# Kernel optimization log

Measured on AMD Instinct MI355X. Metric: run time of the kernel, lower is better.

The kernel has to match this reference:

```python
import jax, jax.numpy as jnp
import numpy as np

WS = 7          # window size
DIM = 192
HEADS = 6
NW = 64         # number of windows per image (mask leading dim)
NC = 3          # n_contrast (q and kv)
B_ = 1024       # num_windows * batch


def _relative_position_index(ws):
    coords = np.stack(np.meshgrid(np.arange(ws), np.arange(ws), indexing='ij'))  # (2, ws, ws)
    cf = coords.reshape(2, -1)                       # (2, ws*ws)
    rel = cf[:, :, None] - cf[:, None, :]            # (2, N, N)
    rel = rel.transpose(1, 2, 0).copy()              # (N, N, 2)
    rel[:, :, 0] += ws - 1
    rel[:, :, 1] += ws - 1
    rel[:, :, 0] *= 2 * ws - 1
    return rel.sum(-1)                               # (N, N) int

REL_IDX = jnp.asarray(_relative_position_index(WS))


def setup_inputs() -> dict:
    key = jax.random.key(0)
    ks = jax.random.split(key, 13)
    f32 = jnp.float32
    inp = {
        'x_q': jax.random.normal(ks[0], (B_, NC, WS, WS, DIM), f32),
        'x_k': jax.random.normal(ks[1], (B_, NC, WS, WS, DIM), f32),
        'x_v': jax.random.normal(ks[2], (B_, NC, WS, WS, DIM), f32),
        'mask': jax.random.normal(ks[3], (NW, WS * WS, WS * WS), f32),
        # Linear weights stored torch-style: (out_features, in_features)
        'q_w': jax.random.normal(ks[4], (DIM, DIM), f32) * 0.02,
        'q_b': jnp.zeros((DIM,), f32),
        'k_w': jax.random.normal(ks[5], (DIM, DIM), f32) * 0.02,
        'k_b': jnp.zeros((DIM,), f32),
        'v_w': jax.random.normal(ks[6], (DIM, DIM), f32) * 0.02,
        'v_b': jnp.zeros((DIM,), f32),
        'proj_w': jax.random.normal(ks[7], (DIM, DIM), f32) * 0.02,
        'proj_b': jnp.zeros((DIM,), f32),
        'bias_table': jax.random.normal(ks[8], ((2 * WS - 1) ** 2, HEADS), f32) * 0.02,
    }
    return inp


def reference(x_q, x_k, x_v, mask, q_w, q_b, k_w, k_b, v_w, v_b, proj_w, proj_b, bias_table):
    Bw, ncq, Wh, Ww, C = x_q.shape
    nckv = x_k.shape[1]
    H = HEADS
    hd = C // H
    Nq = ncq * Wh * Ww
    Nkv = nckv * Wh * Ww

    xq = x_q.reshape(Bw, Nq, C)
    xk = x_k.reshape(Bw, Nkv, C)
    xv = x_v.reshape(Bw, Nkv, C)

    q = (xq @ q_w.T + q_b).reshape(Bw, Nq, H, hd).transpose(0, 2, 1, 3)   # (B_, H, Nq, hd)
    k = (xk @ k_w.T + k_b).reshape(Bw, Nkv, H, hd).transpose(0, 2, 1, 3)
    v = (xv @ v_w.T + v_b).reshape(Bw, Nkv, H, hd).transpose(0, 2, 1, 3)

    scale = hd ** (-0.5)
    attn = jnp.einsum('bhqd,bhkd->bhqk', q * scale, k)                    # (B_, H, Nq, Nkv)

    Nwin = Wh * Ww
    bias = bias_table[REL_IDX.reshape(-1)].reshape(Nwin, Nwin, H)
    bias = bias.transpose(2, 0, 1)                                        # (H, Nwin, Nwin)
    bias = jnp.tile(bias, (1, ncq, nckv))                                 # (H, Nq, Nkv)
    attn = attn + bias[None]

    nW = mask.shape[0]
    m = jnp.tile(mask, (1, ncq, nckv))                                    # (nW, Nq, Nkv)
    attn = attn.reshape(Bw // nW, nW, H, Nq, Nkv) + m[None, :, None]
    attn = attn.reshape(Bw, H, Nq, Nkv)
    attn = jax.nn.softmax(attn, axis=-1)

    out = jnp.einsum('bhqk,bhkd->bhqd', attn, v)                          # (B_, H, Nq, hd)
    out = out.transpose(0, 2, 1, 3).reshape(Bw, Nq, C)
    out = out @ proj_w.T + proj_b
    return out.reshape(Bw, ncq, Wh, Ww, C)
```

## Files before the change

### kernel.cpp

```cpp
#include <hip/hip_runtime.h>
#include <stdint.h>

#define ROWS 150528
#define QSCALE 0.17677669529663687f
#define L2E 1.44269504088896f

typedef __attribute__((ext_vector_type(8))) __bf16 bf16x8;
typedef __attribute__((ext_vector_type(4))) __bf16 bf16x4;
typedef __attribute__((ext_vector_type(4))) float f32x4;
typedef __attribute__((ext_vector_type(4))) float f4;

static __device__ __forceinline__ f32x4 mfma_bf16(bf16x8 a, bf16x8 b, f32x4 c) {
  return __builtin_amdgcn_mfma_f32_16x16x32_bf16(a, b, c, 0, 0, 0);
}

static __device__ __forceinline__ uint32_t pack_bf16(float a, float b) {
  uint16_t ux = __builtin_bit_cast(uint16_t, (__bf16)a);
  uint16_t uy = __builtin_bit_cast(uint16_t, (__bf16)b);
  return (uint32_t)ux | ((uint32_t)uy << 16);
}

#define GLOAD_LDS16(gp, lp)                                                     \
  __builtin_amdgcn_global_load_lds(                                             \
      (const __attribute__((address_space(1))) uint32_t*)(gp),                  \
      (__attribute__((address_space(3))) uint32_t*)(lp), 16, 0, 0)

__global__ void prep(const float* __restrict__ q_w, const float* __restrict__ k_w,
                     const float* __restrict__ v_w, const float* __restrict__ p_w,
                     __bf16* __restrict__ wq, __bf16* __restrict__ wk,
                     __bf16* __restrict__ wv, __bf16* __restrict__ wp,
                     const float* __restrict__ maskp, const float* __restrict__ btab,
                     float* __restrict__ bmall) {
  const int bid = blockIdx.x;
  if (bid < 144) {
    const int y = bid / 36;
    const float* s = y == 0 ? q_w : y == 1 ? k_w : y == 2 ? v_w : p_w;
    __bf16* d = y == 0 ? wq : y == 1 ? wk : y == 2 ? wv : wp;
    int i = (bid % 36) * 256 + threadIdx.x;
    f4 v = ((const f4*)s)[i];
    bf16x4 b;
    b[0] = (__bf16)v[0]; b[1] = (__bf16)v[1]; b[2] = (__bf16)v[2]; b[3] = (__bf16)v[3];
    ((bf16x4*)d)[i] = b;
  } else {
    const int idx = bid - 144;
    const int win = idx / 6, h = idx - win * 6;
    float* dst = bmall + ((size_t)idx) * 2800;
    for (int i = threadIdx.x; i < 2796; i += 256) {
      int q = i / 57, ke = i - q * 57;
      int k = ke >= 49 ? ke - 49 : ke;
      if (q > 48) q = 48;
      int qi = q / 7, qj = q - qi * 7, ki = k / 7, kj = k - ki * 7;
      int rel = (qi - ki + 6) * 13 + (qj - kj + 6);
      dst[i] = (maskp[win * 2401 + q * 49 + k] + btab[rel * 6 + h]) * L2E;
    }
  }
}

template<bool IN_F32, bool OUT_F32, int RPT, int TILES>
static __device__ __forceinline__
void gemm_pipe(const void* __restrict__ Xv, const __bf16* __restrict__ Wb,
               const float* __restrict__ bias, void* __restrict__ Ov, float scale,
               char* Xs)
{
  constexpr int CPR = IN_F32 ? 48 : 24;
  constexpr int LPW = RPT * CPR / 256;
  constexpr int TB  = RPT * CPR * 16;
  constexpr int RG  = RPT / 16;
  constexpr int STEADY = RG * 12 + LPW;
  const int tid = threadIdx.x;
  const int wv = tid >> 6, lane = tid & 63, lr = lane & 15, lg = lane >> 4;
  const size_t blk0 = (size_t)blockIdx.x * (RPT * TILES);

  bf16x8 wf[3][6];
  float bcol[3];
  #pragma unroll
  for (int t = 0; t < 3; ++t) {
    const int nt = wv + 4 * t;
    const __bf16* wr = &Wb[(nt * 16 + lr) * 192 + lg * 8];
    #pragma unroll
    for (int kk = 0; kk < 6; ++kk) wf[t][kk] = *(const bf16x8*)&wr[kk * 32];
    bcol[t] = bias[nt * 16 + lr] * scale;
  }

  auto stage = [&](int buf, int t) {
    const size_t row0 = blk0 + (size_t)t * RPT;
    char* ldsb = Xs + buf * TB;
    int l = (wv * LPW) * 64 + lane;
    #pragma unroll
    for (int p = 0; p < LPW; ++p) {
      int r = l / CPR;
      int c16 = (l - r * CPR) ^ (r & 7);
      const char* src;
      if (IN_F32) {
        src = (const char*)Xv + ((row0 + r) * 768 + c16 * 16);
      } else {
        int hh = c16 >> 2, sub = c16 & 3;
        src = (const char*)Xv + (((size_t)hh * ROWS + row0 + r) * 64 + sub * 16);
      }
      GLOAD_LDS16(src, ldsb + (wv * LPW + p) * 1024);
      l += 64;
    }
  };

  stage(0, 0);
  stage(1, 1);

  #pragma unroll
  for (int it = 0; it < TILES; ++it) {
    if (it == 0) {
      asm volatile("s_waitcnt vmcnt(%0)" :: "i"(LPW) : "memory");
    } else if (it + 1 < TILES) {
      asm volatile("s_waitcnt vmcnt(%0)" :: "i"(STEADY) : "memory");
    } else {
      asm volatile("s_waitcnt vmcnt(0)" ::: "memory");
    }
    __builtin_amdgcn_s_barrier();

    const size_t row0 = blk0 + (size_t)it * RPT;
    const char* cb = Xs + (it % 3) * TB;

    bf16x8 a[RG][6];
    #pragma unroll
    for (int rg = 0; rg < RG; ++rg) {
      const int rr = rg * 16 + lr;
      const char* rb = cb + rr * (CPR * 16);
      const int sw = rr & 7;
      if (IN_F32) {
        #pragma unroll
        for (int kk = 0; kk < 6; ++kk) {
          const int g0 = kk * 8 + lg * 2;
          f4 lo = *(const f4*)(rb + ((g0 ^ sw) * 16));
          f4 hi = *(const f4*)(rb + (((g0 + 1) ^ sw) * 16));
          #pragma unroll
          for (int e = 0; e < 4; ++e) {
            a[rg][kk][e]     = (__bf16)lo[e];
            a[rg][kk][4 + e] = (__bf16)hi[e];
          }
        }
      } else {
        #pragma unroll
        for (int kk = 0; kk < 6; ++kk) {
          const int g = kk * 4 + lg;
          a[rg][kk] = *(const bf16x8*)(rb + ((g ^ sw) * 16));
        }
      }
    }

    if (it + 2 < TILES) stage((it + 2) % 3, it + 2);
    asm volatile("" ::: "memory");

    #pragma unroll
    for (int rg = 0; rg < RG; ++rg) {
      const size_t grow = row0 + rg * 16 + lg * 4;
      #pragma unroll
      for (int t = 0; t < 3; ++t) {
        f32x4 acc = {0.f, 0.f, 0.f, 0.f};
        #pragma unroll
        for (int kk = 0; kk < 6; ++kk) acc = mfma_bf16(a[rg][kk], wf[t][kk], acc);
        const int nt = wv + 4 * t;
        if (OUT_F32) {
          const int col = nt * 16 + lr;
          #pragma unroll
          for (int j = 0; j < 4; ++j)
            ((float*)Ov)[(grow + j) * 192 + col] = acc[j] * scale + bcol[t];
        } else {
          const int hh = nt >> 1, c32 = (nt & 1) * 16 + lr;
          #pragma unroll
          for (int j = 0; j < 4; ++j)
            ((__bf16*)Ov)[((size_t)hh * ROWS + grow + j) * 32 + c32] =
                (__bf16)(acc[j] * scale + bcol[t]);
        }
      }
    }
    asm volatile("" ::: "memory");
  }
}

__global__ __launch_bounds__(256, 2)
void qkvgemm(const float* __restrict__ xq, const float* __restrict__ xk,
             const float* __restrict__ xv,
             const __bf16* __restrict__ wq, const __bf16* __restrict__ wk,
             const __bf16* __restrict__ wv,
             const float* __restrict__ bq, const float* __restrict__ bk,
             const float* __restrict__ bv,
             __bf16* __restrict__ oq, __bf16* __restrict__ ok,
             __bf16* __restrict__ ov)
{
  __shared__ __align__(16) char Xs[3 * 12288];
  const int y = blockIdx.y;
  const float* x = y == 0 ? xq : y == 1 ? xk : xv;
  const __bf16* w = y == 0 ? wq : y == 1 ? wk : wv;
  const float* bi = y == 0 ? bq : y == 1 ? bk : bv;
  __bf16* o = y == 0 ? oq : y == 1 ? ok : ov;
  const float scale = y == 0 ? (QSCALE * L2E) : 1.f;
  gemm_pipe<true, false, 16, 8>(x, w, bi, o, scale, Xs);
}

__global__ __launch_bounds__(256, 2)
void projgemm(const __bf16* __restrict__ X, const __bf16* __restrict__ Wb,
              const float* __restrict__ bias, float* __restrict__ Ov)
{
  __shared__ __align__(16) char Xs[3 * 12288];
  gemm_pipe<false, true, 32, 6>(X, Wb, bias, Ov, 1.f, Xs);
}

__global__ __launch_bounds__(320, 5)
void attn8(const __bf16* __restrict__ Q, const __bf16* __restrict__ K,
           const __bf16* __restrict__ V, __bf16* __restrict__ O,
           const float* __restrict__ bmall)
{
  __shared__ __align__(16) __bf16 Ks[160 * 40];
  __shared__ __align__(16) __bf16 Vt[32 * 168];
  __shared__ __align__(16) float bm2[2796];

  const int b = blockIdx.x, h = blockIdx.y;
  const int tid = threadIdx.x;
  const size_t hb = (size_t)h * ROWS + (size_t)b * 147;
  const int wv = tid >> 6, lane = tid & 63;
  const int lr = lane & 15, lg = lane >> 4;

  bf16x8 qf = *(const bf16x8*)&Q[(hb + wv * 16 + lr) * 32 + lg * 8];

  {
    const f4* bsrc = (const f4*)(bmall + (size_t)((b & 63) * 6 + h) * 2800);
    for (int i = tid; i < 699; i += 320) ((f4*)bm2)[i] = bsrc[i];
  }
  for (int i = tid; i < 588; i += 320) {
    int k = i >> 2, c = i & 3;
    int phys = (k & ~31) | (((k >> 2) & 1) << 4) | (((k >> 3) & 3) << 2) | (k & 3);
    *(bf16x8*)&Ks[phys * 40 + c * 8] = *(const bf16x8*)&K[(hb + k) * 32 + c * 8];
  }
  for (int t = tid; t < 588; t += 320) {
    int key = t >> 2, dblk = t & 3;
    bf16x8 v = *(const bf16x8*)&V[(hb + key) * 32 + dblk * 8];
    #pragma unroll
    for (int e = 0; e < 8; ++e) Vt[(dblk * 8 + e) * 168 + key] = v[e];
  }
  for (int i = tid; i < 32 * 13; i += 320) {
    int d = i / 13, key = 147 + (i - (i / 13) * 13);
    Vt[d * 168 + key] = (__bf16)0.f;
  }
  __syncthreads();

  #pragma unroll
  for (int t = 0; t < 2; ++t) {
    const int mt = wv + 5 * t;

    bf16x8 qn = qf;
    if (t == 0) {
      int qr = (wv + 5) * 16 + lr; if (qr > 146) qr = 146;
      qn = *(const bf16x8*)&Q[(hb + qr) * 32 + lg * 8];
    }

    int r = mt * 16 + lr;
    int q49 = r; if (q49 >= 98) q49 -= 98; if (q49 >= 49) q49 -= 49;
    const float* bmrow = &bm2[q49 * 57];

    f32x4 o0 = {0.f,0.f,0.f,0.f}, o1 = {0.f,0.f,0.f,0.f};
    float sum = 0.f;
    int kb = lg * 8;
    #pragma unroll
    for (int s = 0; s < 5; ++s) {
      const f32x4 z = {0.f,0.f,0.f,0.f};
      f32x4 st0 = mfma_bf16(*(const bf16x8*)&Ks[(s * 32 + lr) * 40 + lg * 8], qf, z);
      f32x4 st1 = mfma_bf16(*(const bf16x8*)&Ks[(s * 32 + 16 + lr) * 40 + lg * 8], qf, z);
      const float* bp = bmrow + kb;
      #pragma unroll
      for (int j = 0; j < 4; ++j) { st0[j] += bp[j]; st1[j] += bp[4 + j]; }
      if (s == 4) {
        #pragma unroll
        for (int j = 0; j < 4; ++j) {
          if (lg * 8 + j >= 19) st0[j] = -1e30f;
          if (lg * 8 + j >= 15) st1[j] = -1e30f;
        }
      }
      #pragma unroll
      for (int j = 0; j < 4; ++j) { st0[j] = exp2f(st0[j]); sum += st0[j]; }
      #pragma unroll
      for (int j = 0; j < 4; ++j) { st1[j] = exp2f(st1[j]); sum += st1[j]; }
      union { bf16x8 v; uint32_t w[4]; } pu;
      pu.w[0] = pack_bf16(st0[0], st0[1]);
      pu.w[1] = pack_bf16(st0[2], st0[3]);
      pu.w[2] = pack_bf16(st1[0], st1[1]);
      pu.w[3] = pack_bf16(st1[2], st1[3]);
      bf16x8 v0 = *(const bf16x8*)&Vt[lr * 168 + s * 32 + lg * 8];
      bf16x8 v1 = *(const bf16x8*)&Vt[(16 + lr) * 168 + s * 32 + lg * 8];
      o0 = mfma_bf16(pu.v, v0, o0);
      o1 = mfma_bf16(pu.v, v1, o1);
      kb += 32; if (kb >= 49) kb -= 49;
    }
    sum += __shfl_xor(sum, 16);
    sum += __shfl_xor(sum, 32);
    const float rinv = 1.f / sum;
    #pragma unroll
    for (int j = 0; j < 4; ++j) {
      const int qa = mt * 16 + lg * 4 + j;
      const float rj = __shfl(rinv, lg * 4 + j);
      if (qa < 147) {
        const size_t base = (hb + qa) * 32;
        O[base + lr]      = (__bf16)(o0[j] * rj);
        O[base + 16 + lr] = (__bf16)(o1[j] * rj);
      }
    }
    qf = qn;
  }
}

extern "C" void kernel_launch(void* const* d_in, const int* in_sizes, int n_in,
                              void* d_out, int out_size, void* d_ws, size_t ws_size,
                              hipStream_t stream) {
  (void)in_sizes; (void)n_in; (void)out_size;
  const float* x_q  = (const float*)d_in[0];
  const float* x_k  = (const float*)d_in[1];
  const float* x_v  = (const float*)d_in[2];
  const float* maskp= (const float*)d_in[3];
  const float* q_w  = (const float*)d_in[4];
  const float* q_b  = (const float*)d_in[5];
  const float* k_w  = (const float*)d_in[6];
  const float* k_b  = (const float*)d_in[7];
  const float* v_w  = (const float*)d_in[8];
  const float* v_b  = (const float*)d_in[9];
  const float* p_w  = (const float*)d_in[10];
  const float* p_b  = (const float*)d_in[11];
  const float* btab = (const float*)d_in[12];

  char* ws = (char*)d_ws;
  float* bmall = (float*)ws;
  const size_t bmsz = (size_t)64 * 6 * 2800 * sizeof(float);
  char* wsp = ws + bmsz;
  const size_t wsz = 36864 * sizeof(__bf16);
  __bf16* wq  = (__bf16*)wsp;
  __bf16* wk  = (__bf16*)(wsp + wsz);
  __bf16* wvp = (__bf16*)(wsp + 2 * wsz);
  __bf16* wp  = (__bf16*)(wsp + 3 * wsz);
  char* bufs = wsp + 4 * wsz;
  const size_t sz = (size_t)ROWS * 192 * sizeof(__bf16);
  __bf16* qb = (__bf16*)bufs;
  __bf16* kb = (__bf16*)(bufs + sz);
  __bf16* vb = (__bf16*)(bufs + 2 * sz);
  const size_t need4 = bmsz + 4 * wsz + 4 * sz;
  __bf16* ob = (ws_size >= need4) ? (__bf16*)(bufs + 3 * sz) : qb;

  prep<<<528, 256, 0, stream>>>(q_w, k_w, v_w, p_w, wq, wk, wvp, wp,
                                maskp, btab, bmall);

  qkvgemm<<<dim3(ROWS / 128, 3), 256, 0, stream>>>(x_q, x_k, x_v, wq, wk, wvp,
                                                   q_b, k_b, v_b, qb, kb, vb);

  attn8<<<dim3(1024, 6), 320, 0, stream>>>(qb, kb, vb, ob, bmall);

  projgemm<<<ROWS / 192, 256, 0, stream>>>(ob, wp, p_b, (float*)d_out);
}
```

Before: 261.7 us.

## Transpose GEMM MFMA output for vector stores, remap blocks across XCDs, relax waitcnt

The GEMM MFMA operands are swapped so each lane holds four consecutive output columns of one row. Bias and output stores become 16-byte float4 or 8-byte packed bf16 writes instead of scalar strided ones. Block indices in all three kernels are remapped so consecutive row ranges land on the same XCD (8-way interleave), aiming at better L2 locality. The vmcnt waits are recomputed to count the new, fewer store instructions, which adds risk if the counts are wrong.

```diff
diff --git a/kernel.cpp b/kernel.cpp
--- a/kernel.cpp
+++ b/kernel.cpp
@@ -9,6 +9,7 @@
 typedef __attribute__((ext_vector_type(4))) __bf16 bf16x4;
 typedef __attribute__((ext_vector_type(4))) float f32x4;
 typedef __attribute__((ext_vector_type(4))) float f4;
+typedef __attribute__((ext_vector_type(2))) uint32_t u32x2;
 
 static __device__ __forceinline__ f32x4 mfma_bf16(bf16x8 a, bf16x8 b, f32x4 c) {
   return __builtin_amdgcn_mfma_f32_16x16x32_bf16(a, b, c, 0, 0, 0);
@@ -60,26 +61,28 @@
 static __device__ __forceinline__
 void gemm_pipe(const void* __restrict__ Xv, const __bf16* __restrict__ Wb,
                const float* __restrict__ bias, void* __restrict__ Ov, float scale,
-               char* Xs)
+               char* Xs, int bx)
 {
   constexpr int CPR = IN_F32 ? 48 : 24;
   constexpr int LPW = RPT * CPR / 256;
   constexpr int TB  = RPT * CPR * 16;
   constexpr int RG  = RPT / 16;
-  constexpr int STEADY = RG * 12 + LPW;
+  constexpr int SPT = RG * 3;
   const int tid = threadIdx.x;
   const int wv = tid >> 6, lane = tid & 63, lr = lane & 15, lg = lane >> 4;
-  const size_t blk0 = (size_t)blockIdx.x * (RPT * TILES);
+  const size_t blk0 = (size_t)bx * (RPT * TILES);
 
   bf16x8 wf[3][6];
-  float bcol[3];
+  f4 bc4[3];
   #pragma unroll
   for (int t = 0; t < 3; ++t) {
     const int nt = wv + 4 * t;
     const __bf16* wr = &Wb[(nt * 16 + lr) * 192 + lg * 8];
     #pragma unroll
     for (int kk = 0; kk < 6; ++kk) wf[t][kk] = *(const bf16x8*)&wr[kk * 32];
-    bcol[t] = bias[nt * 16 + lr] * scale;
+    f4 bb = *(const f4*)&bias[nt * 16 + 4 * lg];
+    #pragma unroll
+    for (int e = 0; e < 4; ++e) bc4[t][e] = bb[e] * scale;
   }
 
   auto stage = [&](int buf, int t) {
@@ -109,10 +112,12 @@
   for (int it = 0; it < TILES; ++it) {
     if (it == 0) {
       asm volatile("s_waitcnt vmcnt(%0)" :: "i"(LPW) : "memory");
+    } else if (it == 1) {
+      asm volatile("s_waitcnt vmcnt(%0)" :: "i"(SPT + LPW) : "memory");
     } else if (it + 1 < TILES) {
-      asm volatile("s_waitcnt vmcnt(%0)" :: "i"(STEADY) : "memory");
+      asm volatile("s_waitcnt vmcnt(%0)" :: "i"(2 * SPT + LPW) : "memory");
     } else {
-      asm volatile("s_waitcnt vmcnt(0)" ::: "memory");
+      asm volatile("s_waitcnt vmcnt(%0)" :: "i"(2 * SPT) : "memory");
     }
     __builtin_amdgcn_s_barrier();
 
@@ -151,24 +156,25 @@
 
     #pragma unroll
     for (int rg = 0; rg < RG; ++rg) {
-      const size_t grow = row0 + rg * 16 + lg * 4;
+      const size_t grow = row0 + rg * 16 + lr;
       #pragma unroll
       for (int t = 0; t < 3; ++t) {
         f32x4 acc = {0.f, 0.f, 0.f, 0.f};
         #pragma unroll
-        for (int kk = 0; kk < 6; ++kk) acc = mfma_bf16(a[rg][kk], wf[t][kk], acc);
+        for (int kk = 0; kk < 6; ++kk) acc = mfma_bf16(wf[t][kk], a[rg][kk], acc);
         const int nt = wv + 4 * t;
         if (OUT_F32) {
-          const int col = nt * 16 + lr;
+          f4 ov;
           #pragma unroll
-          for (int j = 0; j < 4; ++j)
-            ((float*)Ov)[(grow + j) * 192 + col] = acc[j] * scale + bcol[t];
+          for (int j = 0; j < 4; ++j) ov[j] = acc[j] * scale + bc4[t][j];
+          *(f4*)&((float*)Ov)[grow * 192 + nt * 16 + 4 * lg] = ov;
         } else {
-          const int hh = nt >> 1, c32 = (nt & 1) * 16 + lr;
-          #pragma unroll
-          for (int j = 0; j < 4; ++j)
-            ((__bf16*)Ov)[((size_t)hh * ROWS + grow + j) * 32 + c32] =
-                (__bf16)(acc[j] * scale + bcol[t]);
+          u32x2 pw;
+          pw[0] = pack_bf16(acc[0] * scale + bc4[t][0], acc[1] * scale + bc4[t][1]);
+          pw[1] = pack_bf16(acc[2] * scale + bc4[t][2], acc[3] * scale + bc4[t][3]);
+          const int hh = nt >> 1;
+          *(u32x2*)&((__bf16*)Ov)[((size_t)hh * ROWS + grow) * 32 +
+                                  (nt & 1) * 16 + 4 * lg] = pw;
         }
       }
     }
@@ -188,12 +194,13 @@
 {
   __shared__ __align__(16) char Xs[3 * 12288];
   const int y = blockIdx.y;
+  const int bx = (blockIdx.x & 7) * 147 + (blockIdx.x >> 3);
   const float* x = y == 0 ? xq : y == 1 ? xk : xv;
   const __bf16* w = y == 0 ? wq : y == 1 ? wk : wv;
   const float* bi = y == 0 ? bq : y == 1 ? bk : bv;
   __bf16* o = y == 0 ? oq : y == 1 ? ok : ov;
   const float scale = y == 0 ? (QSCALE * L2E) : 1.f;
-  gemm_pipe<true, false, 16, 8>(x, w, bi, o, scale, Xs);
+  gemm_pipe<true, false, 16, 8>(x, w, bi, o, scale, Xs, bx);
 }
 
 __global__ __launch_bounds__(256, 2)
@@ -201,7 +208,8 @@
               const float* __restrict__ bias, float* __restrict__ Ov)
 {
   __shared__ __align__(16) char Xs[3 * 12288];
-  gemm_pipe<false, true, 32, 6>(X, Wb, bias, Ov, 1.f, Xs);
+  const int bx = (blockIdx.x & 7) * 98 + (blockIdx.x >> 3);
+  gemm_pipe<false, true, 32, 6>(X, Wb, bias, Ov, 1.f, Xs, bx);
 }
 
 __global__ __launch_bounds__(320, 5)
@@ -213,7 +221,8 @@
   __shared__ __align__(16) __bf16 Vt[32 * 168];
   __shared__ __align__(16) float bm2[2796];
 
-  const int b = blockIdx.x, h = blockIdx.y;
+  const int b = (blockIdx.x & 7) * 128 + (blockIdx.x >> 3);
+  const int h = blockIdx.y;
   const int tid = threadIdx.x;
   const size_t hb = (size_t)h * ROWS + (size_t)b * 147;
   const int wv = tid >> 6, lane = tid & 63;
```

Measured after the change: 260.3 us. Within noise of the previous version (-0.5%).
